# Optimization experiments

Measured on AMD Instinct MI355X. Metric: run time of the kernel, lower is better.

## Reference

```python
import jax, jax.numpy as jnp
import numpy as np

N = 100_000       # total nodes
E = 1_600_000     # edges (avg degree 16)
IN, H, L = 16, 64, 32
G = 100           # graphs
NPG = N // G      # nodes per graph (equal-sized graphs)


def _glorot(key, fan_in, fan_out):
    s = np.sqrt(6.0 / (fan_in + fan_out)).astype(np.float32)
    return jax.random.uniform(key, (fan_in, fan_out), jnp.float32, -s, s)


def setup_inputs() -> dict:
    key = jax.random.key(0)
    ks = jax.random.split(key, 6)
    x = jax.random.normal(ks[0], (N, IN), jnp.float32)
    edge_index = jax.random.randint(ks[1], (2, E), 0, N, dtype=jnp.int64)
    batch = jnp.repeat(jnp.arange(G, dtype=jnp.int64), NPG)  # sorted graph ids
    kw = jax.random.split(ks[2], 4)
    return dict(
        x=x, edge_index=edge_index, batch=batch, nodes_per_graph=NPG,
        W1=_glorot(kw[0], IN, H), b1=jnp.zeros((H,), jnp.float32),
        W2=_glorot(kw[1], H, L), b2=jnp.zeros((L,), jnp.float32),
        W3=_glorot(kw[2], L, H), b3=jnp.zeros((H,), jnp.float32),
        W4=_glorot(kw[3], H, IN), b4=jnp.zeros((IN,), jnp.float32),
    )


def _gcn(x, W, b, src, dst, norm, n):
    # GCNConv: out[dst] += norm_e * (x @ W)[src], plus bias
    h = x @ W
    msg = h[src] * norm[:, None]
    return jax.ops.segment_sum(msg, dst, num_segments=n) + b


def reference(x, edge_index, batch, nodes_per_graph,
              W1, b1, W2, b2, W3, b3, W4, b4):
    n = x.shape[0]
    loops = jnp.arange(n, dtype=edge_index.dtype)
    src = jnp.concatenate([edge_index[0], loops])  # add self-loops (PyG default)
    dst = jnp.concatenate([edge_index[1], loops])
    deg = jax.ops.segment_sum(jnp.ones_like(dst, jnp.float32), dst, num_segments=n)
    dis = jax.lax.rsqrt(jnp.maximum(deg, 1.0))  # deg >= 1 from self-loops
    norm = dis[src] * dis[dst]                   # symmetric normalization

    # encode
    h = jax.nn.relu(_gcn(x, W1, b1, src, dst, norm, n))
    h = _gcn(h, W2, b2, src, dst, norm, n)
    g = n // nodes_per_graph
    sums = jax.ops.segment_sum(h, batch, num_segments=g)
    cnts = jax.ops.segment_sum(jnp.ones((n, 1), jnp.float32), batch, num_segments=g)
    z = sums / cnts                              # global_mean_pool -> [G, L]

    # decode: repeat_interleave(bincount(batch)) with equal graph sizes
    zr = jnp.repeat(z, nodes_per_graph, axis=0)  # [N, L]
    d = jax.nn.relu(_gcn(zr, W3, b3, src, dst, norm, n))
    return _gcn(d, W4, b4, src, dst, norm, n)    # [N, IN]
```

## Files before the change

### kernel.cpp

```cpp
#include <hip/hip_runtime.h>
#include <hip/hip_bf16.h>
#include <hip/hip_fp16.h>


constexpr int BSZ_LOG = 9;
constexpr int BSZ     = 1 << BSZ_LOG;
constexpr int NBMAX   = 256;
constexpr int ECHUNK  = 8192;
constexpr int BCAP    = 12288;
constexpr int ZSPLIT  = 8;

struct alignas(8) h4 { __half2 a, b; };

__device__ __forceinline__ float4 h4_to_f4(h4 v) {
    float2 fa = __half22float2(v.a), fb = __half22float2(v.b);
    return make_float4(fa.x, fa.y, fb.x, fb.y);
}

__device__ __forceinline__ int gdiv(int v, int npg, float inv) {
    int g = __float2int_rz((float)v * inv);
    int r = v - g * npg;
    if (r < 0) --g; else if (r >= npg) ++g;
    return g;
}

__global__ __launch_bounds__(256)
void binfill_kernel(const int* __restrict__ src, const int* __restrict__ dst,
                    int* __restrict__ bcnt, int* __restrict__ binned, int E) {
    __shared__ int hist[NBMAX], hexcl[NBMAX], gbase[NBMAX], hpos[NBMAX], tmp[NBMAX];
    __shared__ int sorted[ECHUNK];
    __shared__ unsigned char bsorted[ECHUNK];
    int t = threadIdx.x;
    hist[t] = 0; hpos[t] = 0;
    __syncthreads();
    int e0 = blockIdx.x * ECHUNK;
    int cnt = min(ECHUNK, E - e0);
    for (int i = t; i < cnt; i += 256)
        atomicAdd(&hist[dst[e0 + i] >> BSZ_LOG], 1);
    __syncthreads();
    tmp[t] = hist[t];
    __syncthreads();
    for (int d = 1; d < 256; d <<= 1) {
        int v = (t >= d) ? tmp[t - d] : 0;
        __syncthreads();
        tmp[t] += v;
        __syncthreads();
    }
    hexcl[t] = (t == 0) ? 0 : tmp[t - 1];
    int h = hist[t];
    gbase[t] = (h > 0) ? atomicAdd(&bcnt[t], h) : 0;
    __syncthreads();
    for (int i = t; i < cnt; i += 256) {
        int s = src[e0 + i], d = dst[e0 + i];
        int b = d >> BSZ_LOG;
        int code = ((d & (BSZ - 1)) << 20) | s;
        int sp = hexcl[b] + atomicAdd(&hpos[b], 1);
        sorted[sp] = code;
        bsorted[sp] = (unsigned char)b;
    }
    __syncthreads();
    for (int i = t; i < cnt; i += 256) {
        int b = bsorted[i];
        binned[(size_t)b * BCAP + gbase[b] + (i - hexcl[b])] = sorted[i];
    }
}

__device__ __forceinline__ int prefix_before(const int* __restrict__ bcnt,
                                             int b, int* sums) {
    int t = threadIdx.x;
    sums[t] = (t < b) ? bcnt[t] : 0;
    __syncthreads();
    for (int d = 128; d > 0; d >>= 1) {
        if (t < d) sums[t] += sums[t + d];
        __syncthreads();
    }
    int r = sums[0];
    __syncthreads();
    return r;
}

__global__ __launch_bounds__(256)
void csr_off_kernel(const int* __restrict__ binned, const int* __restrict__ bcnt,
                    int* __restrict__ off, float* __restrict__ dis,
                    int* __restrict__ lstart_g, int* __restrict__ bstart_g,
                    int n, int E) {
    __shared__ int hist[BSZ];
    __shared__ int lstart[BSZ];
    __shared__ int partial[256];
    int b = blockIdx.x, t = threadIdx.x;
    int nb0 = b << BSZ_LOG;
    int nn = min(BSZ, n - nb0);
    int m = bcnt[b];
    int bs = prefix_before(bcnt, b, partial);
    const int* bp = binned + (size_t)b * BCAP;
    for (int i = t; i < BSZ; i += 256) hist[i] = 0;
    __syncthreads();
    for (int i = t; i < m; i += 256)
        atomicAdd(&hist[bp[i] >> 20], 1);
    __syncthreads();
    int a0 = hist[2 * t], a1 = hist[2 * t + 1];
    partial[t] = a0 + a1;
    __syncthreads();
    for (int d = 1; d < 256; d <<= 1) {
        int v = (t >= d) ? partial[t - d] : 0;
        __syncthreads();
        partial[t] += v;
        __syncthreads();
    }
    int base = (t == 0) ? 0 : partial[t - 1];
    lstart[2 * t] = base;
    lstart[2 * t + 1] = base + a0;
    __syncthreads();
    for (int i = t; i < BSZ; i += 256)
        lstart_g[(b << BSZ_LOG) + i] = lstart[i];
    for (int i = t; i < nn; i += 256) {
        off[nb0 + i] = bs + lstart[i];
        dis[nb0 + i] = rsqrtf((float)hist[i] + 1.0f);
    }
    if (t == 0) bstart_g[b] = bs;
    if (b == 0 && t == 0) off[n] = E;
}

__global__ __launch_bounds__(256)
void bucket_scatter_kernel(const int* __restrict__ binned, const int* __restrict__ bcnt,
                           const int* __restrict__ lstart_g, const int* __restrict__ bstart_g,
                           const float* __restrict__ dis,
                           const int* __restrict__ npg_p, int2* __restrict__ ew, int n) {
    __shared__ int lstart[BSZ];
    __shared__ int lpos[BSZ];
    __shared__ float ldis[BSZ];
    int b = blockIdx.x, t = threadIdx.x;
    int nb0 = b << BSZ_LOG;
    int nn = min(BSZ, n - nb0);
    int m = bcnt[b];
    int e0 = bstart_g[b];
    int npg = npg_p[0];
    float inv = 1.0f / (float)npg;
    const int* bp = binned + (size_t)b * BCAP;
    for (int i = t; i < BSZ; i += 256) {
        lstart[i] = lstart_g[(b << BSZ_LOG) + i];
        lpos[i] = 0;
        ldis[i] = (i < nn) ? dis[nb0 + i] : 0.f;
    }
    __syncthreads();
    for (int i = t; i < m; i += 256) {
        int code = bp[i];
        int dl = code >> 20, s = code & 0xFFFFF;
        float w = dis[s] * ldis[dl];
        int g = gdiv(s, npg, inv);
        int p = e0 + lstart[dl] + atomicAdd(&lpos[dl], 1);
        ew[p] = make_int2(s | (g << 20), __float_as_int(w));
    }
}

__global__ __launch_bounds__(256)
void xconv_kernel(const float* __restrict__ x, h4* __restrict__ xh, int n4) {
    const float4* xp = (const float4*)x;
    for (int i = blockIdx.x * 256 + threadIdx.x; i < n4; i += gridDim.x * 256) {
        float4 v = xp[i];
        h4 o;
        o.a = __floats2half2_rn(v.x, v.y);
        o.b = __floats2half2_rn(v.z, v.w);
        xh[i] = o;
    }
}

template <int TPN, bool USE_G>
__device__ __forceinline__ float4
edge_loop_h(const h4* __restrict__ hp, const int2* __restrict__ ew,
            int e0, int e1, int q, float4 acc) {
    int deg = e1 - e0;
    int nfull = deg / TPN;
    int r = deg - nfull * TPN;
    int idx = e0 + q;
    int2 a = make_int2(0, 0);
    if (idx < e1) a = ew[idx];
    for (int c = 0; c < nfull; ++c) {
        int nidx = idx + (c + 1) * TPN;
        int2 an = make_int2(0, 0);
        if (nidx < e1) an = ew[nidx];
#pragma unroll
        for (int k = 0; k < TPN; ++k) {
            int ax = __shfl(a.x, k, TPN);
            float w = __int_as_float(__shfl(a.y, k, TPN));
            int row = USE_G ? (int)(((unsigned)ax) >> 20) : (ax & 0xFFFFF);
            float4 v = h4_to_f4(hp[(size_t)row * TPN + q]);
            acc.x += w * v.x; acc.y += w * v.y; acc.z += w * v.z; acc.w += w * v.w;
        }
        a = an;
    }
    for (int k = 0; k < r; ++k) {
        int ax = __shfl(a.x, k, TPN);
        float w = __int_as_float(__shfl(a.y, k, TPN));
        int row = USE_G ? (int)(((unsigned)ax) >> 20) : (ax & 0xFFFFF);
        float4 v = h4_to_f4(hp[(size_t)row * TPN + q]);
        acc.x += w * v.x; acc.y += w * v.y; acc.z += w * v.z; acc.w += w * v.w;
    }
    return acc;
}

template <int TPN, bool USE_G>
__device__ __forceinline__ float4
edge_loop(const float4* __restrict__ hp, const int2* __restrict__ ew,
          int e0, int e1, int q, float4 acc) {
    int deg = e1 - e0;
    int nfull = deg / TPN;
    int r = deg - nfull * TPN;
    int idx = e0 + q;
    int2 a = make_int2(0, 0);
    if (idx < e1) a = ew[idx];
    for (int c = 0; c < nfull; ++c) {
        int nidx = idx + (c + 1) * TPN;
        int2 an = make_int2(0, 0);
        if (nidx < e1) an = ew[nidx];
#pragma unroll
        for (int k = 0; k < TPN; ++k) {
            int ax = __shfl(a.x, k, TPN);
            float w = __int_as_float(__shfl(a.y, k, TPN));
            int row = USE_G ? (int)(((unsigned)ax) >> 20) : (ax & 0xFFFFF);
            float4 v = hp[(size_t)row * TPN + q];
            acc.x += w * v.x; acc.y += w * v.y; acc.z += w * v.z; acc.w += w * v.w;
        }
        a = an;
    }
    for (int k = 0; k < r; ++k) {
        int ax = __shfl(a.x, k, TPN);
        float w = __int_as_float(__shfl(a.y, k, TPN));
        int row = USE_G ? (int)(((unsigned)ax) >> 20) : (ax & 0xFFFFF);
        float4 v = hp[(size_t)row * TPN + q];
        acc.x += w * v.x; acc.y += w * v.y; acc.z += w * v.z; acc.w += w * v.w;
    }
    return acc;
}

__global__ __launch_bounds__(256)
void l1w2_kernel(const h4* __restrict__ xh, const float* __restrict__ dis,
                 const int* __restrict__ off, const int2* __restrict__ ew,
                 const float* __restrict__ W1, const float* __restrict__ b1,
                 const float* __restrict__ W2, __half* __restrict__ t2h, int n) {
    __shared__ float accs[64][17];
    __shared__ __half2 hlh[64][33];
    __shared__ float Wl[16 * 64];
    __shared__ float bl[64];
    int t = threadIdx.x;
    for (int i = t; i < 16 * 64; i += 256) Wl[i] = W1[i];
    if (t < 64) bl[t] = b1[t];

    int q = t & 3, ln = t >> 2;
    int node = blockIdx.x * 64 + ln;
    float4 acc = make_float4(0.f, 0.f, 0.f, 0.f);
    if (node < n) {
        float di = dis[node], d2 = di * di;
        float4 v = h4_to_f4(xh[(size_t)node * 4 + q]);
        acc.x = d2 * v.x; acc.y = d2 * v.y; acc.z = d2 * v.z; acc.w = d2 * v.w;
        acc = edge_loop_h<4, false>(xh, ew, off[node], off[node + 1], q, acc);
    }
    accs[ln][q * 4 + 0] = acc.x; accs[ln][q * 4 + 1] = acc.y;
    accs[ln][q * 4 + 2] = acc.z; accs[ln][q * 4 + 3] = acc.w;
    __syncthreads();

    int j = t & 63;
    for (int nb = (t >> 6); nb < 64; nb += 4) {
        float s = bl[j];
#pragma unroll
        for (int k = 0; k < 16; ++k) s += accs[nb][k] * Wl[k * 64 + j];
        float h = fmaxf(s, 0.f);
        ((__half*)hlh[nb])[j] = __float2half(h);
    }
    __syncthreads();

    int base = blockIdx.x * 64;
    int c = t & 31;
    for (int nb = (t >> 5); nb < 64; nb += 8) {
        int nd = base + nb;
        if (nd >= n) break;
        float s = 0.f;
#pragma unroll
        for (int k = 0; k < 32; ++k) {
            float2 hp = __half22float2(hlh[nb][k]);
            s += hp.x * W2[(2 * k) * 32 + c] + hp.y * W2[(2 * k + 1) * 32 + c];
        }
        t2h[(size_t)nd * 32 + c] = __float2half(s);
    }
}

__global__ __launch_bounds__(256)
void agg16h_kernel(const h4* __restrict__ t4h, const float* __restrict__ dis,
                   const int* __restrict__ off, const int2* __restrict__ ew,
                   const float* __restrict__ b, float* __restrict__ out, int n) {
    int t = threadIdx.x;
    int q = t & 3, ln = t >> 2;
    int node = blockIdx.x * 64 + ln;
    if (node >= n) return;
    float di = dis[node], d2 = di * di;
    float4 v = h4_to_f4(t4h[(size_t)node * 4 + q]);
    float4 acc;
    acc.x = d2 * v.x; acc.y = d2 * v.y; acc.z = d2 * v.z; acc.w = d2 * v.w;
    acc = edge_loop_h<4, false>(t4h, ew, off[node], off[node + 1], q, acc);
    float4 bb = ((const float4*)b)[q];
    float4 o;
    o.x = acc.x + bb.x; o.y = acc.y + bb.y; o.z = acc.z + bb.z; o.w = acc.w + bb.w;
    ((float4*)out)[(size_t)node * 4 + q] = o;
}

__global__ __launch_bounds__(256)
void zagg_kernel(const h4* __restrict__ t2h, const float* __restrict__ dis,
                 const int* __restrict__ off, const int2* __restrict__ ew,
                 const int* __restrict__ npg_p, float* __restrict__ zsum, int n) {
    __shared__ float4 red0[256];
    __shared__ float4 red1[256];
    int blk = blockIdx.x;
    int b = blk / ZSPLIT, s = blk % ZSPLIT;
    int t = threadIdx.x, q = t & 7, r = t >> 3;
    int npg = npg_p[0];
    int nb0 = b << BSZ_LOG;
    int nn = min(BSZ, n - nb0);
    int g0 = nb0 / npg;
    int nodeB = min((g0 + 1) * npg - nb0, nn);
    int e0 = off[nb0], e1 = off[nb0 + nn];
    int P  = off[nb0 + nodeB];
    int m = e1 - e0;

    float4 a0 = make_float4(0.f, 0.f, 0.f, 0.f);
    float4 a1 = make_float4(0.f, 0.f, 0.f, 0.f);
    int i0 = (int)((long long)m * s / ZSPLIT);
    int i1 = (int)((long long)m * (s + 1) / ZSPLIT);
    for (int i = i0 + r; i < i1; i += 32) {
        int e = e0 + i;
        int2 aa = ew[e];
        float w = __int_as_float(aa.y);
        int src = aa.x & 0xFFFFF;
        float4 v = h4_to_f4(t2h[(size_t)src * 8 + q]);
        if (e < P) {
            a0.x += w * v.x; a0.y += w * v.y; a0.z += w * v.z; a0.w += w * v.w;
        } else {
            a1.x += w * v.x; a1.y += w * v.y; a1.z += w * v.z; a1.w += w * v.w;
        }
    }
    int j0 = nn * s / ZSPLIT, j1 = nn * (s + 1) / ZSPLIT;
    for (int i = j0 + r; i < j1; i += 32) {
        int node = nb0 + i;
        float di = dis[node], d2 = di * di;
        float4 v = h4_to_f4(t2h[(size_t)node * 8 + q]);
        if (i < nodeB) {
            a0.x += d2 * v.x; a0.y += d2 * v.y; a0.z += d2 * v.z; a0.w += d2 * v.w;
        } else {
            a1.x += d2 * v.x; a1.y += d2 * v.y; a1.z += d2 * v.z; a1.w += d2 * v.w;
        }
    }
    red0[t] = a0; red1[t] = a1;
    __syncthreads();
    for (int d = 128; d >= 8; d >>= 1) {
        if (t < d) {
            float4 u = red0[t], v = red0[t + d];
            u.x += v.x; u.y += v.y; u.z += v.z; u.w += v.w;
            red0[t] = u;
            u = red1[t]; v = red1[t + d];
            u.x += v.x; u.y += v.y; u.z += v.z; u.w += v.w;
            red1[t] = u;
        }
        __syncthreads();
    }
    if (t < 8) {
        float4 v = red0[t];
        atomicAdd(&zsum[g0 * 32 + t * 4 + 0], v.x);
        atomicAdd(&zsum[g0 * 32 + t * 4 + 1], v.y);
        atomicAdd(&zsum[g0 * 32 + t * 4 + 2], v.z);
        atomicAdd(&zsum[g0 * 32 + t * 4 + 3], v.w);
    } else if (t < 16 && nodeB < nn) {
        float4 v = red1[t - 8];
        atomicAdd(&zsum[(g0 + 1) * 32 + (t - 8) * 4 + 0], v.x);
        atomicAdd(&zsum[(g0 + 1) * 32 + (t - 8) * 4 + 1], v.y);
        atomicAdd(&zsum[(g0 + 1) * 32 + (t - 8) * 4 + 2], v.z);
        atomicAdd(&zsum[(g0 + 1) * 32 + (t - 8) * 4 + 3], v.w);
    }
}

__global__ __launch_bounds__(256)
void zred_kernel(const float* __restrict__ zsum, const float* __restrict__ b2,
                 const int* __restrict__ npg_p, float* __restrict__ Z, int n) {
    int npg = npg_p[0];
    int G = n / npg;
    float inv = 1.0f / (float)npg;
    for (int i = blockIdx.x * 256 + threadIdx.x; i < G * 32; i += gridDim.x * 256)
        Z[i] = zsum[i] * inv + b2[i & 31];
}

__global__ __launch_bounds__(256)
void dec1v4_kernel(const float* __restrict__ Z, const float* __restrict__ dis,
                   const int* __restrict__ off, const int2* __restrict__ ew,
                   const int* __restrict__ npg_p, const float* __restrict__ W3,
                   const float* __restrict__ b3, const float* __restrict__ W4,
                   __half* __restrict__ t4h, int n) {
    __shared__ float zacc[32 * 36];
    __shared__ float hl[32 * 68];
    int t = threadIdx.x;
    int npg = npg_p[0];
    float inv = 1.0f / (float)npg;
    int q = t & 7, ln = t >> 3;
    int base = blockIdx.x * 32;
    int node = base + ln;
    const float4* zp = (const float4*)Z;

    float4 acc = make_float4(0.f, 0.f, 0.f, 0.f);
    if (node < n) {
        float di = dis[node], d2 = di * di;
        int gi = gdiv(node, npg, inv);
        float4 v = zp[(size_t)gi * 8 + q];
        acc.x = d2 * v.x; acc.y = d2 * v.y; acc.z = d2 * v.z; acc.w = d2 * v.w;
        acc = edge_loop<8, true>(zp, ew, off[node], off[node + 1], q, acc);
    }
    zacc[ln * 36 + q * 4 + 0] = acc.x;
    zacc[ln * 36 + q * 4 + 1] = acc.y;
    zacc[ln * 36 + q * 4 + 2] = acc.z;
    zacc[ln * 36 + q * 4 + 3] = acc.w;
    __syncthreads();

    {
        int j = t & 63;
        int i0 = (t >> 6) * 8;
        float w3c[32];
#pragma unroll
        for (int k = 0; k < 32; ++k) w3c[k] = W3[k * 64 + j];
        float bj = b3[j];
        const float4* za4 = (const float4*)zacc;
#pragma unroll
        for (int ii = 0; ii < 8; ++ii) {
            int i = i0 + ii;
            float s = bj;
#pragma unroll
            for (int m = 0; m < 8; ++m) {
                float4 zv = za4[i * 9 + m];
                s += zv.x * w3c[4 * m] + zv.y * w3c[4 * m + 1]
                   + zv.z * w3c[4 * m + 2] + zv.w * w3c[4 * m + 3];
            }
            hl[i * 68 + j] = fmaxf(s, 0.f);
        }
    }
    __syncthreads();

    {
        int c = t & 15;
        int i0 = t >> 4;
        int i1 = i0 + 16;
        const float4* hl4 = (const float4*)hl;
        float s0 = 0.f, s1 = 0.f;
#pragma unroll
        for (int kh = 0; kh < 2; ++kh) {
            float w4c[32];
#pragma unroll
            for (int k = 0; k < 32; ++k) w4c[k] = W4[(kh * 32 + k) * 16 + c];
#pragma unroll
            for (int m = 0; m < 8; ++m) {
                float4 h0 = hl4[i0 * 17 + kh * 8 + m];
                float4 h1 = hl4[i1 * 17 + kh * 8 + m];
                s0 += h0.x * w4c[4 * m] + h0.y * w4c[4 * m + 1]
                    + h0.z * w4c[4 * m + 2] + h0.w * w4c[4 * m + 3];
                s1 += h1.x * w4c[4 * m] + h1.y * w4c[4 * m + 1]
                    + h1.z * w4c[4 * m + 2] + h1.w * w4c[4 * m + 3];
            }
        }
        int nd0 = base + i0, nd1 = base + i1;
        if (nd0 < n) t4h[(size_t)nd0 * 16 + c] = __float2half(s0);
        if (nd1 < n) t4h[(size_t)nd1 * 16 + c] = __float2half(s1);
    }
}

extern "C" void kernel_launch(void* const* d_in, const int* in_sizes, int n_in,
                              void* d_out, int out_size, void* d_ws, size_t ws_size,
                              hipStream_t stream) {
    const float* x     = (const float*)d_in[0];
    const int*   ei    = (const int*)d_in[1];
    const int*   npg   = (const int*)d_in[3];
    const float* W1 = (const float*)d_in[4];
    const float* b1 = (const float*)d_in[5];
    const float* W2 = (const float*)d_in[6];
    const float* b2 = (const float*)d_in[7];
    const float* W3 = (const float*)d_in[8];
    const float* b3 = (const float*)d_in[9];
    const float* W4 = (const float*)d_in[10];
    const float* b4 = (const float*)d_in[11];
    float* out = (float*)d_out;

    int n = in_sizes[0] / 16;
    int E = in_sizes[1] / 2;
    const int* srcp = ei;
    const int* dstp = ei + E;

    char* w = (char*)d_ws;
    auto alloc = [&](size_t bytes) {
        char* p = w;
        w += (bytes + 255) & ~(size_t)255;
        return p;
    };
    float*  dis      = (float*)alloc((size_t)n * 4);
    int*    off      = (int*)alloc(((size_t)n + 1) * 4);
    int*    binned   = (int*)alloc((size_t)NBMAX * BCAP * 4);
    int2*   ew       = (int2*)alloc((size_t)E * 8);
    h4*     xh       = (h4*)alloc((size_t)n * 16 * 2);
    __half* t2h      = (__half*)alloc((size_t)n * 32 * 2);
    __half* t4h      = (__half*)alloc((size_t)n * 16 * 2);
    float*  Z        = (float*)alloc((size_t)4096 * 32 * 4);
    float*  zsum     = (float*)alloc((size_t)4096 * 32 * 4);
    int*    bcnt     = (int*)alloc((size_t)NBMAX * 4);
    int*    lstart_g = (int*)alloc((size_t)NBMAX * BSZ * 4);
    int*    bstart_g = (int*)alloc((size_t)NBMAX * 4);

    int nbuck = (n + BSZ - 1) / BSZ;
    int nbin  = (E + ECHUNK - 1) / ECHUNK;

    hipMemsetAsync(bcnt, 0, (size_t)NBMAX * 4, stream);
    hipMemsetAsync(zsum, 0, (size_t)4096 * 32 * 4, stream);
    xconv_kernel<<<512, 256, 0, stream>>>(x, xh, n * 4);
    binfill_kernel<<<nbin, 256, 0, stream>>>(srcp, dstp, bcnt, binned, E);
    csr_off_kernel<<<nbuck, 256, 0, stream>>>(binned, bcnt, off, dis, lstart_g, bstart_g, n, E);
    bucket_scatter_kernel<<<nbuck, 256, 0, stream>>>(binned, bcnt, lstart_g, bstart_g, dis, npg, ew, n);

    l1w2_kernel<<<(n + 63) / 64, 256, 0, stream>>>(xh, dis, off, ew, W1, b1, W2, t2h, n);
    zagg_kernel<<<nbuck * ZSPLIT, 256, 0, stream>>>((const h4*)t2h, dis, off, ew, npg, zsum, n);
    zred_kernel<<<16, 256, 0, stream>>>(zsum, b2, npg, Z, n);

    dec1v4_kernel<<<(n + 31) / 32, 256, 0, stream>>>(Z, dis, off, ew, npg, W3, b3, W4, t4h, n);
    agg16h_kernel<<<(n + 63) / 64, 256, 0, stream>>>((const h4*)t4h, dis, off, ew, b4, out, n);
}
```

Measured before the change: 200.8 us.

## Factor symmetric GCN normalization into node scaling, shrink per-edge records to int

Uses the factorization norm = dis[src]*dis[dst]. Source features are pre-scaled by dis[src] when they are produced (xconv, t2h, t4h), and the destination scale is applied once after aggregation. This lets the l1 and final aggregation loops drop the per-edge weight and read only a 4-byte index instead of an 8-byte int2. The zagg and decoder paths, which aggregate unscaled data, instead read separate fp16 per-edge dis arrays. This cuts edge-stream bandwidth and shuffle work, but adds two half arrays and fp16 rounding of the weights.

```diff
diff --git a/kernel.cpp b/kernel.cpp
--- a/kernel.cpp
+++ b/kernel.cpp
@@ -125,7 +125,8 @@
 void bucket_scatter_kernel(const int* __restrict__ binned, const int* __restrict__ bcnt,
                            const int* __restrict__ lstart_g, const int* __restrict__ bstart_g,
                            const float* __restrict__ dis,
-                           const int* __restrict__ npg_p, int2* __restrict__ ew, int n) {
+                           const int* __restrict__ npg_p, int* __restrict__ ew4,
+                           __half* __restrict__ diss, __half* __restrict__ disw, int n) {
     __shared__ int lstart[BSZ];
     __shared__ int lpos[BSZ];
     __shared__ float ldis[BSZ];
@@ -146,96 +147,94 @@
     for (int i = t; i < m; i += 256) {
         int code = bp[i];
         int dl = code >> 20, s = code & 0xFFFFF;
-        float w = dis[s] * ldis[dl];
         int g = gdiv(s, npg, inv);
         int p = e0 + lstart[dl] + atomicAdd(&lpos[dl], 1);
-        ew[p] = make_int2(s | (g << 20), __float_as_int(w));
-    }
-}
-
-__global__ __launch_bounds__(256)
-void xconv_kernel(const float* __restrict__ x, h4* __restrict__ xh, int n4) {
+        ew4[p]  = s | (g << 20);
+        diss[p] = __float2half(dis[s]);
+        disw[p] = __float2half(ldis[dl]);
+    }
+}
+
+__global__ __launch_bounds__(256)
+void xconv_kernel(const float* __restrict__ x, const float* __restrict__ dis,
+                  h4* __restrict__ xh, int n4) {
     const float4* xp = (const float4*)x;
     for (int i = blockIdx.x * 256 + threadIdx.x; i < n4; i += gridDim.x * 256) {
+        float d = dis[i >> 2];
         float4 v = xp[i];
         h4 o;
-        o.a = __floats2half2_rn(v.x, v.y);
-        o.b = __floats2half2_rn(v.z, v.w);
+        o.a = __floats2half2_rn(d * v.x, d * v.y);
+        o.b = __floats2half2_rn(d * v.z, d * v.w);
         xh[i] = o;
     }
 }
 
-template <int TPN, bool USE_G>
+template <int TPN>
 __device__ __forceinline__ float4
-edge_loop_h(const h4* __restrict__ hp, const int2* __restrict__ ew,
-            int e0, int e1, int q, float4 acc) {
+edge_loop_ns(const h4* __restrict__ hp, const int* __restrict__ ew4,
+             int e0, int e1, int q, float4 acc) {
     int deg = e1 - e0;
     int nfull = deg / TPN;
     int r = deg - nfull * TPN;
     int idx = e0 + q;
-    int2 a = make_int2(0, 0);
-    if (idx < e1) a = ew[idx];
+    int a = (idx < e1) ? ew4[idx] : 0;
     for (int c = 0; c < nfull; ++c) {
         int nidx = idx + (c + 1) * TPN;
-        int2 an = make_int2(0, 0);
-        if (nidx < e1) an = ew[nidx];
+        int an = (nidx < e1) ? ew4[nidx] : 0;
 #pragma unroll
         for (int k = 0; k < TPN; ++k) {
-            int ax = __shfl(a.x, k, TPN);
-            float w = __int_as_float(__shfl(a.y, k, TPN));
-            int row = USE_G ? (int)(((unsigned)ax) >> 20) : (ax & 0xFFFFF);
+            int ax = __shfl(a, k, TPN);
+            int row = ax & 0xFFFFF;
             float4 v = h4_to_f4(hp[(size_t)row * TPN + q]);
+            acc.x += v.x; acc.y += v.y; acc.z += v.z; acc.w += v.w;
+        }
+        a = an;
+    }
+    for (int k = 0; k < r; ++k) {
+        int ax = __shfl(a, k, TPN);
+        int row = ax & 0xFFFFF;
+        float4 v = h4_to_f4(hp[(size_t)row * TPN + q]);
+        acc.x += v.x; acc.y += v.y; acc.z += v.z; acc.w += v.w;
+    }
+    return acc;
+}
+
+__device__ __forceinline__ float4
+zedge_loop(const float4* __restrict__ zp, const int* __restrict__ ew4,
+           const __half* __restrict__ diss, int e0, int e1, int q, float4 acc) {
+    int deg = e1 - e0;
+    int nfull = deg / 8;
+    int r = deg - nfull * 8;
+    int idx = e0 + q;
+    int a = 0; float wq = 0.f;
+    if (idx < e1) { a = ew4[idx]; wq = __half2float(diss[idx]); }
+    for (int c = 0; c < nfull; ++c) {
+        int nidx = idx + (c + 1) * 8;
+        int an = 0; float wn = 0.f;
+        if (nidx < e1) { an = ew4[nidx]; wn = __half2float(diss[nidx]); }
+#pragma unroll
+        for (int k = 0; k < 8; ++k) {
+            int ax = __shfl(a, k, 8);
+            float w = __shfl(wq, k, 8);
+            int g = (int)(((unsigned)ax) >> 20);
+            float4 v = zp[(size_t)g * 8 + q];
             acc.x += w * v.x; acc.y += w * v.y; acc.z += w * v.z; acc.w += w * v.w;
         }
-        a = an;
+        a = an; wq = wn;
     }
     for (int k = 0; k < r; ++k) {
-        int ax = __shfl(a.x, k, TPN);
-        float w = __int_as_float(__shfl(a.y, k, TPN));
-        int row = USE_G ? (int)(((unsigned)ax) >> 20) : (ax & 0xFFFFF);
-        float4 v = h4_to_f4(hp[(size_t)row * TPN + q]);
+        int ax = __shfl(a, k, 8);
+        float w = __shfl(wq, k, 8);
+        int g = (int)(((unsigned)ax) >> 20);
+        float4 v = zp[(size_t)g * 8 + q];
         acc.x += w * v.x; acc.y += w * v.y; acc.z += w * v.z; acc.w += w * v.w;
     }
     return acc;
 }
 
-template <int TPN, bool USE_G>
-__device__ __forceinline__ float4
-edge_loop(const float4* __restrict__ hp, const int2* __restrict__ ew,
-          int e0, int e1, int q, float4 acc) {
-    int deg = e1 - e0;
-    int nfull = deg / TPN;
-    int r = deg - nfull * TPN;
-    int idx = e0 + q;
-    int2 a = make_int2(0, 0);
-    if (idx < e1) a = ew[idx];
-    for (int c = 0; c < nfull; ++c) {
-        int nidx = idx + (c + 1) * TPN;
-        int2 an = make_int2(0, 0);
-        if (nidx < e1) an = ew[nidx];
-#pragma unroll
-        for (int k = 0; k < TPN; ++k) {
-            int ax = __shfl(a.x, k, TPN);
-            float w = __int_as_float(__shfl(a.y, k, TPN));
-            int row = USE_G ? (int)(((unsigned)ax) >> 20) : (ax & 0xFFFFF);
-            float4 v = hp[(size_t)row * TPN + q];
-            acc.x += w * v.x; acc.y += w * v.y; acc.z += w * v.z; acc.w += w * v.w;
-        }
-        a = an;
-    }
-    for (int k = 0; k < r; ++k) {
-        int ax = __shfl(a.x, k, TPN);
-        float w = __int_as_float(__shfl(a.y, k, TPN));
-        int row = USE_G ? (int)(((unsigned)ax) >> 20) : (ax & 0xFFFFF);
-        float4 v = hp[(size_t)row * TPN + q];
-        acc.x += w * v.x; acc.y += w * v.y; acc.z += w * v.z; acc.w += w * v.w;
-    }
-    return acc;
-}
-
 __global__ __launch_bounds__(256)
 void l1w2_kernel(const h4* __restrict__ xh, const float* __restrict__ dis,
-                 const int* __restrict__ off, const int2* __restrict__ ew,
+                 const int* __restrict__ off, const int* __restrict__ ew4,
                  const float* __restrict__ W1, const float* __restrict__ b1,
                  const float* __restrict__ W2, __half* __restrict__ t2h, int n) {
     __shared__ float accs[64][17];
@@ -250,10 +249,11 @@
     int node = blockIdx.x * 64 + ln;
     float4 acc = make_float4(0.f, 0.f, 0.f, 0.f);
     if (node < n) {
-        float di = dis[node], d2 = di * di;
+        float dnode = dis[node];
         float4 v = h4_to_f4(xh[(size_t)node * 4 + q]);
-        acc.x = d2 * v.x; acc.y = d2 * v.y; acc.z = d2 * v.z; acc.w = d2 * v.w;
-        acc = edge_loop_h<4, false>(xh, ew, off[node], off[node + 1], q, acc);
+        acc.x = v.x; acc.y = v.y; acc.z = v.z; acc.w = v.w;
+        acc = edge_loop_ns<4>(xh, ew4, off[node], off[node + 1], q, acc);
+        acc.x *= dnode; acc.y *= dnode; acc.z *= dnode; acc.w *= dnode;
     }
     accs[ln][q * 4 + 0] = acc.x; accs[ln][q * 4 + 1] = acc.y;
     accs[ln][q * 4 + 2] = acc.z; accs[ln][q * 4 + 3] = acc.w;
@@ -264,8 +264,7 @@
         float s = bl[j];
 #pragma unroll
         for (int k = 0; k < 16; ++k) s += accs[nb][k] * Wl[k * 64 + j];
-        float h = fmaxf(s, 0.f);
-        ((__half*)hlh[nb])[j] = __float2half(h);
+        ((__half*)hlh[nb])[j] = __float2half(fmaxf(s, 0.f));
     }
     __syncthreads();
 
@@ -280,32 +279,34 @@
             float2 hp = __half22float2(hlh[nb][k]);
             s += hp.x * W2[(2 * k) * 32 + c] + hp.y * W2[(2 * k + 1) * 32 + c];
         }
-        t2h[(size_t)nd * 32 + c] = __float2half(s);
+        t2h[(size_t)nd * 32 + c] = __float2half(dis[nd] * s);
     }
 }
 
 __global__ __launch_bounds__(256)
 void agg16h_kernel(const h4* __restrict__ t4h, const float* __restrict__ dis,
-                   const int* __restrict__ off, const int2* __restrict__ ew,
+                   const int* __restrict__ off, const int* __restrict__ ew4,
                    const float* __restrict__ b, float* __restrict__ out, int n) {
     int t = threadIdx.x;
     int q = t & 3, ln = t >> 2;
     int node = blockIdx.x * 64 + ln;
     if (node >= n) return;
-    float di = dis[node], d2 = di * di;
+    float dnode = dis[node];
     float4 v = h4_to_f4(t4h[(size_t)node * 4 + q]);
     float4 acc;
-    acc.x = d2 * v.x; acc.y = d2 * v.y; acc.z = d2 * v.z; acc.w = d2 * v.w;
-    acc = edge_loop_h<4, false>(t4h, ew, off[node], off[node + 1], q, acc);
+    acc.x = v.x; acc.y = v.y; acc.z = v.z; acc.w = v.w;
+    acc = edge_loop_ns<4>(t4h, ew4, off[node], off[node + 1], q, acc);
     float4 bb = ((const float4*)b)[q];
     float4 o;
-    o.x = acc.x + bb.x; o.y = acc.y + bb.y; o.z = acc.z + bb.z; o.w = acc.w + bb.w;
+    o.x = dnode * acc.x + bb.x; o.y = dnode * acc.y + bb.y;
+    o.z = dnode * acc.z + bb.z; o.w = dnode * acc.w + bb.w;
     ((float4*)out)[(size_t)node * 4 + q] = o;
 }
 
 __global__ __launch_bounds__(256)
 void zagg_kernel(const h4* __restrict__ t2h, const float* __restrict__ dis,
-                 const int* __restrict__ off, const int2* __restrict__ ew,
+                 const int* __restrict__ off, const int* __restrict__ ew4,
+                 const __half* __restrict__ disw,
                  const int* __restrict__ npg_p, float* __restrict__ zsum, int n) {
     __shared__ float4 red0[256];
     __shared__ float4 red1[256];
@@ -327,9 +328,9 @@
     int i1 = (int)((long long)m * (s + 1) / ZSPLIT);
     for (int i = i0 + r; i < i1; i += 32) {
         int e = e0 + i;
-        int2 aa = ew[e];
-        float w = __int_as_float(aa.y);
-        int src = aa.x & 0xFFFFF;
+        int ax = ew4[e];
+        float w = __half2float(disw[e]);
+        int src = ax & 0xFFFFF;
         float4 v = h4_to_f4(t2h[(size_t)src * 8 + q]);
         if (e < P) {
             a0.x += w * v.x; a0.y += w * v.y; a0.z += w * v.z; a0.w += w * v.w;
@@ -340,12 +341,12 @@
     int j0 = nn * s / ZSPLIT, j1 = nn * (s + 1) / ZSPLIT;
     for (int i = j0 + r; i < j1; i += 32) {
         int node = nb0 + i;
-        float di = dis[node], d2 = di * di;
+        float d = dis[node];
         float4 v = h4_to_f4(t2h[(size_t)node * 8 + q]);
         if (i < nodeB) {
-            a0.x += d2 * v.x; a0.y += d2 * v.y; a0.z += d2 * v.z; a0.w += d2 * v.w;
+            a0.x += d * v.x; a0.y += d * v.y; a0.z += d * v.z; a0.w += d * v.w;
         } else {
-            a1.x += d2 * v.x; a1.y += d2 * v.y; a1.z += d2 * v.z; a1.w += d2 * v.w;
+            a1.x += d * v.x; a1.y += d * v.y; a1.z += d * v.z; a1.w += d * v.w;
         }
     }
     red0[t] = a0; red1[t] = a1;
@@ -388,7 +389,8 @@
 
 __global__ __launch_bounds__(256)
 void dec1v4_kernel(const float* __restrict__ Z, const float* __restrict__ dis,
-                   const int* __restrict__ off, const int2* __restrict__ ew,
+                   const int* __restrict__ off, const int* __restrict__ ew4,
+                   const __half* __restrict__ diss,
                    const int* __restrict__ npg_p, const float* __restrict__ W3,
                    const float* __restrict__ b3, const float* __restrict__ W4,
                    __half* __restrict__ t4h, int n) {
@@ -404,11 +406,13 @@
 
     float4 acc = make_float4(0.f, 0.f, 0.f, 0.f);
     if (node < n) {
-        float di = dis[node], d2 = di * di;
+        float dnode = dis[node];
         int gi = gdiv(node, npg, inv);
         float4 v = zp[(size_t)gi * 8 + q];
-        acc.x = d2 * v.x; acc.y = d2 * v.y; acc.z = d2 * v.z; acc.w = d2 * v.w;
-        acc = edge_loop<8, true>(zp, ew, off[node], off[node + 1], q, acc);
+        acc.x = dnode * v.x; acc.y = dnode * v.y;
+        acc.z = dnode * v.z; acc.w = dnode * v.w;
+        acc = zedge_loop(zp, ew4, diss, off[node], off[node + 1], q, acc);
+        acc.x *= dnode; acc.y *= dnode; acc.z *= dnode; acc.w *= dnode;
     }
     zacc[ln * 36 + q * 4 + 0] = acc.x;
     zacc[ln * 36 + q * 4 + 1] = acc.y;
@@ -461,8 +465,8 @@
             }
         }
         int nd0 = base + i0, nd1 = base + i1;
-        if (nd0 < n) t4h[(size_t)nd0 * 16 + c] = __float2half(s0);
-        if (nd1 < n) t4h[(size_t)nd1 * 16 + c] = __float2half(s1);
+        if (nd0 < n) t4h[(size_t)nd0 * 16 + c] = __float2half(dis[nd0] * s0);
+        if (nd1 < n) t4h[(size_t)nd1 * 16 + c] = __float2half(dis[nd1] * s1);
     }
 }
 
@@ -496,7 +500,9 @@
     float*  dis      = (float*)alloc((size_t)n * 4);
     int*    off      = (int*)alloc(((size_t)n + 1) * 4);
     int*    binned   = (int*)alloc((size_t)NBMAX * BCAP * 4);
-    int2*   ew       = (int2*)alloc((size_t)E * 8);
+    int*    ew4      = (int*)alloc((size_t)E * 4);
+    __half* diss     = (__half*)alloc((size_t)E * 2);
+    __half* disw     = (__half*)alloc((size_t)E * 2);
     h4*     xh       = (h4*)alloc((size_t)n * 16 * 2);
     __half* t2h      = (__half*)alloc((size_t)n * 32 * 2);
     __half* t4h      = (__half*)alloc((size_t)n * 16 * 2);
@@ -511,15 +517,16 @@
 
     hipMemsetAsync(bcnt, 0, (size_t)NBMAX * 4, stream);
     hipMemsetAsync(zsum, 0, (size_t)4096 * 32 * 4, stream);
-    xconv_kernel<<<512, 256, 0, stream>>>(x, xh, n * 4);
     binfill_kernel<<<nbin, 256, 0, stream>>>(srcp, dstp, bcnt, binned, E);
     csr_off_kernel<<<nbuck, 256, 0, stream>>>(binned, bcnt, off, dis, lstart_g, bstart_g, n, E);
-    bucket_scatter_kernel<<<nbuck, 256, 0, stream>>>(binned, bcnt, lstart_g, bstart_g, dis, npg, ew, n);
-
-    l1w2_kernel<<<(n + 63) / 64, 256, 0, stream>>>(xh, dis, off, ew, W1, b1, W2, t2h, n);
-    zagg_kernel<<<nbuck * ZSPLIT, 256, 0, stream>>>((const h4*)t2h, dis, off, ew, npg, zsum, n);
+    xconv_kernel<<<512, 256, 0, stream>>>(x, dis, xh, n * 4);
+    bucket_scatter_kernel<<<nbuck, 256, 0, stream>>>(binned, bcnt, lstart_g, bstart_g,
+                                                     dis, npg, ew4, diss, disw, n);
+
+    l1w2_kernel<<<(n + 63) / 64, 256, 0, stream>>>(xh, dis, off, ew4, W1, b1, W2, t2h, n);
+    zagg_kernel<<<nbuck * ZSPLIT, 256, 0, stream>>>((const h4*)t2h, dis, off, ew4, disw, npg, zsum, n);
     zred_kernel<<<16, 256, 0, stream>>>(zsum, b2, npg, Z, n);
 
-    dec1v4_kernel<<<(n + 31) / 32, 256, 0, stream>>>(Z, dis, off, ew, npg, W3, b3, W4, t4h, n);
-    agg16h_kernel<<<(n + 63) / 64, 256, 0, stream>>>((const h4*)t4h, dis, off, ew, b4, out, n);
-}
+    dec1v4_kernel<<<(n + 31) / 32, 256, 0, stream>>>(Z, dis, off, ew4, diss, npg, W3, b3, W4, t4h, n);
+    agg16h_kernel<<<(n + 63) / 64, 256, 0, stream>>>((const h4*)t4h, dis, off, ew4, b4, out, n);
+}
```

Measured after the change: 211.9 us. 1.06x slower.
